# Optimization experiments

Measured on AMD Instinct MI355X. Metric: run time of the kernel, lower is better.

Reference implementation:

```python
import jax, jax.numpy as jnp
import numpy as np

B, S, E, H, FF = 4, 1024, 1024, 16, 4096
D = E // H
EPS = 1e-5


def layer_norm(x, g, b):
    m = jnp.mean(x, axis=-1, keepdims=True)
    v = jnp.var(x, axis=-1, keepdims=True)
    return (x - m) / jnp.sqrt(v + EPS) * g + b


def setup_inputs() -> dict:
    key = jax.random.key(0)
    ks = jax.random.split(key, 12)
    x = jax.random.normal(ks[0], (B, S, E), dtype=jnp.float32)
    # binary attention mask [B,S,S]; force diagonal=1 so no row is fully masked
    mask = jax.random.randint(ks[1], (B, S, S), 0, 2).astype(jnp.float32)
    idx = jnp.arange(S)
    mask = mask.at[:, idx, idx].set(1.0)
    gnn_adj = jax.random.normal(ks[2], (B, S, S), dtype=jnp.float32) * 0.02
    sc = 0.02
    params = dict(
        Wq=jax.random.normal(ks[3], (E, E), dtype=jnp.float32) * sc, bq=jnp.zeros((E,), jnp.float32),
        Wk=jax.random.normal(ks[4], (E, E), dtype=jnp.float32) * sc, bk=jnp.zeros((E,), jnp.float32),
        Wv=jax.random.normal(ks[5], (E, E), dtype=jnp.float32) * sc, bv=jnp.zeros((E,), jnp.float32),
        Wo=jax.random.normal(ks[6], (E, E), dtype=jnp.float32) * sc, bo=jnp.zeros((E,), jnp.float32),
        g1=jnp.ones((E,), jnp.float32), b1=jnp.zeros((E,), jnp.float32),
        g2=jnp.ones((E,), jnp.float32), b2=jnp.zeros((E,), jnp.float32),
        W1=jax.random.normal(ks[7], (E, FF), dtype=jnp.float32) * sc, bf1=jnp.zeros((FF,), jnp.float32),
        W2=jax.random.normal(ks[8], (FF, E), dtype=jnp.float32) * sc, bf2=jnp.zeros((E,), jnp.float32),
    )
    return dict(x=x, mask=mask, gnn_adj=gnn_adj, **params)


def reference(x, mask, gnn_adj, Wq, bq, Wk, bk, Wv, bv, Wo, bo, g1, b1, g2, b2, W1, bf1, W2, bf2):
    # pre-norm (norm_first=True), dropout = identity (eval)
    nx = layer_norm(x, g1, b1)
    # QKV projections -> [B,H,S,D]
    def split_heads(t):
        return t.reshape(B, S, H, D).transpose(0, 2, 1, 3)
    q = split_heads(nx @ Wq + bq)
    k = split_heads(nx @ Wk + bk)
    v = split_heads(nx @ Wv + bv)
    scores = jnp.einsum('bhqd,bhkd->bhqk', q, k) / jnp.sqrt(jnp.float32(D))
    m = mask[:, None]  # [B,1,S,S]
    scores = jnp.where(m == 0, -jnp.inf, scores * m)
    attn = jax.nn.softmax(scores, axis=-1)
    # non-standard: additive bias AFTER softmax
    attn = attn + gnn_adj[:, None]
    xv = jnp.einsum('bhqk,bhkd->bhqd', attn, v)
    xv = xv.transpose(0, 2, 1, 3).reshape(B, S, E)
    x = x + (xv @ Wo + bo)
    h = layer_norm(x, g2, b2)
    ff = jax.nn.gelu(h @ W1 + bf1, approximate=False) @ W2 + bf2
    return x + ff
```

## Files before the change

### kernel.cpp

```cpp
#include <hip/hip_runtime.h>
#include <hip/hip_bf16.h>

typedef unsigned short u16;
typedef short bf16x8 __attribute__((ext_vector_type(8)));
typedef float f32x4 __attribute__((ext_vector_type(4)));

#define B_ 4
#define S_ 1024
#define E_ 1024
#define H_ 16
#define FF_ 4096
#define D_ 64
#define M_ 4096

__device__ __forceinline__ u16 f2bf(float f) {
  unsigned int u = __builtin_bit_cast(unsigned int, f);
  u += 0x7fffu + ((u >> 16) & 1u);
  return (u16)(u >> 16);
}
__device__ __forceinline__ float bf2f(u16 v) {
  unsigned int u = ((unsigned int)v) << 16;
  return __builtin_bit_cast(float, u);
}

__device__ __forceinline__ void gld_lds16(const void* g, void* l) {
  __builtin_amdgcn_global_load_lds((__attribute__((address_space(1))) void*)g,
                                   (__attribute__((address_space(3))) void*)l,
                                   16, 0, 0);
}

__global__ void __launch_bounds__(256) pre_kernel(
    const float* __restrict__ wq, const float* __restrict__ wk,
    const float* __restrict__ wv, const float* __restrict__ wo,
    const float* __restrict__ w1, const float* __restrict__ w2,
    u16* __restrict__ wt,
    const float* __restrict__ x, const float* __restrict__ g1,
    const float* __restrict__ b1, u16* __restrict__ nx,
    const float* __restrict__ mask, const float* __restrict__ gnn,
    u16* __restrict__ biasI, u16* __restrict__ gnnbf) {
  __shared__ __attribute__((aligned(16))) float smem_f[1088];
  int bid = blockIdx.x;
  int t = threadIdx.x;
  if (bid < 12288) {
    const float* src; u16* dst; int K, N; int local;
    if (bid < 4096) {
      int wsel = bid >> 10; local = bid & 1023; K = 1024; N = 1024;
      src = wsel == 0 ? wq : wsel == 1 ? wk : wsel == 2 ? wv : wo;
      dst = wt + (size_t)wsel * 1024 * 1024;
    } else if (bid < 8192) {
      local = bid - 4096; K = 1024; N = 4096; src = w1;
      dst = wt + (size_t)4 * 1024 * 1024;
    } else {
      local = bid - 8192; K = 4096; N = 1024; src = w2;
      dst = wt + (size_t)8 * 1024 * 1024;
    }
    int tiles_n = N >> 5;
    int n0 = (local % tiles_n) << 5, k0 = (local / tiles_n) << 5;
    float (*tl)[33] = reinterpret_cast<float(*)[33]>(smem_f);
    int tx = t & 31, ty = t >> 5;
#pragma unroll
    for (int i = 0; i < 4; ++i)
      tl[ty + i * 8][tx] = src[(size_t)(k0 + ty + i * 8) * N + n0 + tx];
    __syncthreads();
#pragma unroll
    for (int i = 0; i < 4; ++i)
      dst[(size_t)(n0 + ty + i * 8) * K + k0 + tx] = f2bf(tl[tx][ty + i * 8]);
  } else if (bid < 16384) {
    int row = bid - 12288;
    const float* xr = x + (size_t)row * 1024;
    float4 v = *(const float4*)(xr + t * 4);
    float s = v.x + v.y + v.z + v.w;
    float q = v.x * v.x + v.y * v.y + v.z * v.z + v.w * v.w;
#pragma unroll
    for (int off = 1; off < 64; off <<= 1) {
      s += __shfl_xor(s, off);
      q += __shfl_xor(q, off);
    }
    float* sb = smem_f;
    float* qb = smem_f + 4;
    int w = t >> 6, l = t & 63;
    if (l == 0) { sb[w] = s; qb[w] = q; }
    __syncthreads();
    s = sb[0] + sb[1] + sb[2] + sb[3];
    q = qb[0] + qb[1] + qb[2] + qb[3];
    float mean = s * (1.f / 1024.f);
    float var = q * (1.f / 1024.f) - mean * mean;
    float rs = rsqrtf(var + 1e-5f);
    float4 gv = *(const float4*)(g1 + t * 4);
    float4 bv = *(const float4*)(b1 + t * 4);
    ushort4 o;
    o.x = f2bf((v.x - mean) * rs * gv.x + bv.x);
    o.y = f2bf((v.y - mean) * rs * gv.y + bv.y);
    o.z = f2bf((v.z - mean) * rs * gv.z + bv.z);
    o.w = f2bf((v.w - mean) * rs * gv.w + bv.w);
    *(ushort4*)(nx + (size_t)row * 1024 + t * 4) = o;
  } else {
    int row = bid - 16384;
    int b = row >> 10, q = row & 1023;
    float* mrow = smem_f;
    const float* mp = mask + ((size_t)row << 10);
    const float* gp = gnn + ((size_t)row << 10);
    float4 mv = *(const float4*)(mp + t * 4);
    *(float4*)(mrow + t * 4) = mv;
    float4 gv = *(const float4*)(gp + t * 4);
    ushort4 g4;
    g4.x = f2bf(gv.x); g4.y = f2bf(gv.y); g4.z = f2bf(gv.z); g4.w = f2bf(gv.w);
    *(ushort4*)(gnnbf + ((size_t)row << 10) + t * 4) = g4;
    __syncthreads();
    int kt = t >> 4, c = t & 15;
    const u16 NEG = f2bf(-30008.f);
    const u16 SHIFT = f2bf(-8.0f);
    ushort4 o;
    o.x = (mrow[kt * 64 + c] == 0.f) ? NEG : SHIFT;
    o.y = (mrow[kt * 64 + 16 + c] == 0.f) ? NEG : SHIFT;
    o.z = (mrow[kt * 64 + 32 + c] == 0.f) ? NEG : SHIFT;
    o.w = (mrow[kt * 64 + 48 + c] == 0.f) ? NEG : SHIFT;
    *(ushort4*)(biasI + (((size_t)(b * 16 + kt) << 10) + q) * 64 + c * 4) = o;
  }
}

__global__ void __launch_bounds__(256) vtrans_kernel(
    const u16* __restrict__ v, u16* __restrict__ vt) {
  int st = blockIdx.x, h = blockIdx.y, b = blockIdx.z;
  __shared__ u16 tl[64][72];
  const u16* src = v + ((((size_t)(b * 16 + h)) << 10) + (st << 6)) * 64;
  int r = threadIdx.x >> 2, g = (threadIdx.x & 3) << 4;
  *(uint4*)&tl[r][g] = *(const uint4*)(src + r * 64 + g);
  *(uint4*)&tl[r][g + 8] = *(const uint4*)(src + r * 64 + g + 8);
  __syncthreads();
  u16 tmp[16];
#pragma unroll
  for (int i = 0; i < 16; ++i) tmp[i] = tl[g + i][r];
  u16* dst = vt + ((size_t)b << 20) + (((size_t)(h * 64 + r)) << 10) + (st << 6) + g;
  *(uint4*)(dst) = *(uint4*)(tmp);
  *(uint4*)(dst + 8) = *(uint4*)(tmp + 8);
}

__global__ void __launch_bounds__(256) ln_kernel_b(
    const u16* __restrict__ x, const float* __restrict__ g,
    const float* __restrict__ bt, u16* __restrict__ out) {
  int row = blockIdx.x, t = threadIdx.x;
  const u16* xr = x + ((size_t)row << 10);
  ushort4 xv4 = *(const ushort4*)(xr + t * 4);
  float v0 = bf2f(xv4.x), v1 = bf2f(xv4.y), v2 = bf2f(xv4.z), v3 = bf2f(xv4.w);
  float s = v0 + v1 + v2 + v3;
  float q = v0 * v0 + v1 * v1 + v2 * v2 + v3 * v3;
#pragma unroll
  for (int off = 1; off < 64; off <<= 1) {
    s += __shfl_xor(s, off);
    q += __shfl_xor(q, off);
  }
  __shared__ float sb[4], qb[4];
  int w = t >> 6, l = t & 63;
  if (l == 0) { sb[w] = s; qb[w] = q; }
  __syncthreads();
  s = sb[0] + sb[1] + sb[2] + sb[3];
  q = qb[0] + qb[1] + qb[2] + qb[3];
  float mean = s * (1.f / 1024.f);
  float var = q * (1.f / 1024.f) - mean * mean;
  float rs = rsqrtf(var + 1e-5f);
  float4 gv = *(const float4*)(g + t * 4);
  float4 bv = *(const float4*)(bt + t * 4);
  ushort4 o;
  o.x = f2bf((v0 - mean) * rs * gv.x + bv.x);
  o.y = f2bf((v1 - mean) * rs * gv.y + bv.y);
  o.z = f2bf((v2 - mean) * rs * gv.z + bv.z);
  o.w = f2bf((v3 - mean) * rs * gv.w + bv.w);
  *(ushort4*)(out + ((size_t)row << 10) + t * 4) = o;
}

template <int LDA, int LDB, int NKT>
__device__ __forceinline__ void gemm_core_db64(
    const u16* __restrict__ A, const u16* __restrict__ Bt,
    int bm, int bn, u16* lds, f32x4 acc[4][2]) {
  const int tid = threadIdx.x;
  const int w = tid >> 6, l = tid & 63;
  const int wn = w << 5;
  const int lrow = l >> 3;
  const int cg = (l & 7) ^ lrow;
  const u16* Ab = A + (size_t)(bm << 6) * LDA + (cg << 3);
  const u16* Bb = Bt + (size_t)(bn << 7) * LDB + (cg << 3);
#define GSTAGE64(T, BUF)                                                     \
  {                                                                          \
    const int kk = (T) << 6;                                                 \
    u16* la = lds + (BUF) * 12288;                                           \
    u16* lb = la + 4096;                                                     \
    _Pragma("unroll") for (int i = 0; i < 2; ++i) {                          \
      int c = (w << 1) + i;                                                  \
      int row = (c << 3) + lrow;                                             \
      gld_lds16(Ab + (size_t)row * LDA + kk, la + (c << 9));                 \
    }                                                                        \
    _Pragma("unroll") for (int i = 0; i < 4; ++i) {                          \
      int c = (w << 2) + i;                                                  \
      int row = (c << 3) + lrow;                                             \
      gld_lds16(Bb + (size_t)row * LDB + kk, lb + (c << 9));                 \
    }                                                                        \
  }
  GSTAGE64(0, 0);
  __syncthreads();
  for (int t = 0; t < NKT; ++t) {
    if (t + 1 < NKT) GSTAGE64(t + 1, (t & 1) ^ 1);
    const u16* la = lds + (t & 1) * 12288;
    const u16* lb = la + 4096;
    bf16x8 af[2][4], bfr[2][2];
    const int rr = l & 15;
    const int kgb = l >> 4;
#pragma unroll
    for (int ks = 0; ks < 2; ++ks) {
      const int kg = kgb + (ks << 2);
#pragma unroll
      for (int f = 0; f < 4; ++f) {
        int ra = (f << 4) + rr;
        af[ks][f] = *(const bf16x8*)(la + (ra << 6) + ((kg ^ (ra & 7)) << 3));
      }
#pragma unroll
      for (int f = 0; f < 2; ++f) {
        int rb = wn + (f << 4) + rr;
        bfr[ks][f] = *(const bf16x8*)(lb + (rb << 6) + ((kg ^ (rb & 7)) << 3));
      }
    }
#pragma unroll
    for (int fm = 0; fm < 4; ++fm)
#pragma unroll
      for (int fn = 0; fn < 2; ++fn)
#pragma unroll
        for (int ks = 0; ks < 2; ++ks)
          acc[fm][fn] = __builtin_amdgcn_mfma_f32_16x16x32_bf16(
              af[ks][fm], bfr[ks][fn], acc[fm][fn], 0, 0, 0);
    __syncthreads();
  }
#undef GSTAGE64
}

#define ACC_INIT64()                      \
  f32x4 acc[4][2];                        \
  { f32x4 zf = {0.f, 0.f, 0.f, 0.f};      \
_Pragma("unroll")                         \
    for (int a = 0; a < 4; ++a)           \
_Pragma("unroll")                         \
      for (int bb = 0; bb < 2; ++bb) acc[a][bb] = zf; }

#define EPI_SETUP64()                                   \
  const int w = threadIdx.x >> 6, l = threadIdx.x & 63; \
  const int wn = w << 5;

#define GEMM_LDS64() __shared__ __attribute__((aligned(16))) u16 lds[2 * 12288]

__global__ void __launch_bounds__(256, 2) gemm_qkv(
    const u16* __restrict__ nx, const u16* __restrict__ wt,
    const float* __restrict__ bq, const float* __restrict__ bk,
    const float* __restrict__ bv, u16* __restrict__ qk, u16* __restrict__ vtmp) {
  GEMM_LDS64();
  ACC_INIT64();
  int z = blockIdx.z;
  const u16* Bt = wt + (size_t)z * 1024 * 1024;
  const float* bias = z == 0 ? bq : z == 1 ? bk : bv;
  u16* out = z == 2 ? vtmp : qk + (size_t)z * M_ * 1024;
  const float scl = (z == 0) ? 0.18033688f : 1.0f;
  gemm_core_db64<1024, 1024, 16>(nx, Bt, blockIdx.x, blockIdx.y, lds, acc);
  EPI_SETUP64();
#pragma unroll
  for (int fm = 0; fm < 4; ++fm)
#pragma unroll
    for (int fn = 0; fn < 2; ++fn)
#pragma unroll
      for (int j = 0; j < 4; ++j) {
        int row = (blockIdx.x << 6) + (fm << 4) + ((l >> 4) << 2) + j;
        int col = (blockIdx.y << 7) + wn + (fn << 4) + (l & 15);
        float v = (acc[fm][fn][j] + bias[col]) * scl;
        int b = row >> 10, s = row & 1023;
        int h = col >> 6, d = col & 63;
        out[(((size_t)(b * 16 + h) << 10) + s) * 64 + d] = f2bf(v);
      }
}

__global__ void __launch_bounds__(256, 2) gemm_gnnv(
    const u16* __restrict__ gnnbf, const u16* __restrict__ vt,
    u16* __restrict__ xvg) {
  GEMM_LDS64();
  ACC_INIT64();
  int b = blockIdx.z;
  const u16* A = gnnbf + ((size_t)b << 20);
  const u16* Bt = vt + ((size_t)b << 20);
  u16* out = xvg + ((size_t)b << 20);
  gemm_core_db64<1024, 1024, 16>(A, Bt, blockIdx.x, blockIdx.y, lds, acc);
  EPI_SETUP64();
#pragma unroll
  for (int fm = 0; fm < 4; ++fm)
#pragma unroll
    for (int fn = 0; fn < 2; ++fn)
#pragma unroll
      for (int j = 0; j < 4; ++j) {
        int row = (blockIdx.x << 6) + (fm << 4) + ((l >> 4) << 2) + j;
        int col = (blockIdx.y << 7) + wn + (fn << 4) + (l & 15);
        out[((size_t)row << 10) + col] = f2bf(acc[fm][fn][j]);
      }
}

__global__ void __launch_bounds__(256, 2) gemm_wo(
    const u16* __restrict__ xv, const u16* __restrict__ wt,
    const float* __restrict__ bo, const float* __restrict__ xres,
    u16* __restrict__ x1b) {
  GEMM_LDS64();
  ACC_INIT64();
  gemm_core_db64<1024, 1024, 16>(xv, wt, blockIdx.x, blockIdx.y, lds, acc);
  EPI_SETUP64();
#pragma unroll
  for (int fm = 0; fm < 4; ++fm)
#pragma unroll
    for (int fn = 0; fn < 2; ++fn)
#pragma unroll
      for (int j = 0; j < 4; ++j) {
        int row = (blockIdx.x << 6) + (fm << 4) + ((l >> 4) << 2) + j;
        int col = (blockIdx.y << 7) + wn + (fn << 4) + (l & 15);
        size_t idx = ((size_t)row << 10) + col;
        x1b[idx] = f2bf(acc[fm][fn][j] + bo[col] + xres[idx]);
      }
}

__global__ void __launch_bounds__(256, 2) gemm_w1(
    const u16* __restrict__ hb, const u16* __restrict__ wt,
    const float* __restrict__ bf1, u16* __restrict__ ff1) {
  GEMM_LDS64();
  ACC_INIT64();
  gemm_core_db64<1024, 1024, 16>(hb, wt, blockIdx.x, blockIdx.y, lds, acc);
  EPI_SETUP64();
#pragma unroll
  for (int fm = 0; fm < 4; ++fm)
#pragma unroll
    for (int fn = 0; fn < 2; ++fn)
#pragma unroll
      for (int j = 0; j < 4; ++j) {
        int row = (blockIdx.x << 6) + (fm << 4) + ((l >> 4) << 2) + j;
        int col = (blockIdx.y << 7) + wn + (fn << 4) + (l & 15);
        float v = acc[fm][fn][j] + bf1[col];
        float ge = 0.5f * v * (1.f + erff(v * 0.70710678118654752f));
        ff1[((size_t)row << 12) + col] = f2bf(ge);
      }
}

__global__ void __launch_bounds__(256, 2) gemm_w2(
    const u16* __restrict__ ff1, const u16* __restrict__ wt,
    const float* __restrict__ bf2, const u16* __restrict__ x1b,
    float* __restrict__ out) {
  GEMM_LDS64();
  ACC_INIT64();
  gemm_core_db64<4096, 4096, 64>(ff1, wt, blockIdx.x, blockIdx.y, lds, acc);
  EPI_SETUP64();
#pragma unroll
  for (int fm = 0; fm < 4; ++fm)
#pragma unroll
    for (int fn = 0; fn < 2; ++fn)
#pragma unroll
      for (int j = 0; j < 4; ++j) {
        int row = (blockIdx.x << 6) + (fm << 4) + ((l >> 4) << 2) + j;
        int col = (blockIdx.y << 7) + wn + (fn << 4) + (l & 15);
        size_t idx = ((size_t)row << 10) + col;
        out[idx] = acc[fm][fn][j] + bf2[col] + bf2f(x1b[idx]);
      }
}

__global__ void __launch_bounds__(256, 2) attn_kernel(
    const u16* __restrict__ Q, const u16* __restrict__ K,
    const u16* __restrict__ Vt, const u16* __restrict__ biasI,
    const u16* __restrict__ xvg, u16* __restrict__ xv) {
  const int lin = ((blockIdx.x & 7) << 6) + (blockIdx.x >> 3);
  const int qt = lin & 7, h = (lin >> 3) & 15, b = lin >> 7;
  const int tid = threadIdx.x, w = tid >> 6, l = tid & 63;
  __shared__ __attribute__((aligned(16))) u16 kbuf[2][64 * 64];
  __shared__ __attribute__((aligned(16))) u16 vbuf[2][64 * 64];
  __shared__ __attribute__((aligned(16))) u16 pbuf[4][32 * 64];
  const size_t bh = ((size_t)(b * 16 + h)) << 16;
  const u16* Qb = Q + bh;
  const u16* Kb = K + bh;
  const u16* Vtb = Vt + ((size_t)b << 20) + ((size_t)(h * 64) << 10);
  const u16* biasb = biasI + ((size_t)b << 20);
  const int q0 = (qt << 7) + (w << 5);
  const int lrow = l >> 3, cg = (l & 7) ^ lrow;
  const int l4 = l >> 4, lo = l & 15;
  u16* p_w = pbuf[w];

  bf16x8 qf[2][2];
#pragma unroll
  for (int m = 0; m < 2; ++m)
#pragma unroll
    for (int ks = 0; ks < 2; ++ks)
      qf[m][ks] = *(const bf16x8*)(Qb + ((size_t)(q0 + m * 16 + lo) << 6) +
                                   l4 * 8 + ks * 32);
  bf16x8 onesf;
#pragma unroll
  for (int j = 0; j < 8; ++j) onesf[j] = (short)0x3F80;

  f32x4 osoft[2][4], osum[2];
  f32x4 zf = {0.f, 0.f, 0.f, 0.f};
#pragma unroll
  for (int m = 0; m < 2; ++m) {
    osum[m] = zf;
#pragma unroll
    for (int fd = 0; fd < 4; ++fd) osoft[m][fd] = zf;
  }

#define STAGE(T, BUF)                                                          \
  {                                                                            \
    int kv0s = (T) << 6;                                                       \
    u16* kd = &kbuf[BUF][0];                                                   \
    u16* vd = &vbuf[BUF][0];                                                   \
    _Pragma("unroll") for (int i = 0; i < 2; ++i) {                            \
      int c = (w << 1) + i;                                                    \
      gld_lds16(Kb + ((size_t)(kv0s + (c << 3) + lrow) << 6) + (cg << 3),      \
                kd + (c << 9));                                                \
      gld_lds16(Vtb + ((size_t)((c << 3) + lrow) << 10) + kv0s + (cg << 3),    \
                vd + (c << 9));                                                \
    }                                                                          \
  }

  STAGE(0, 0);
  __syncthreads();

  for (int t = 0; t < 16; ++t) {
    const int cur = t & 1;
    if (t < 15) STAGE(t + 1, cur ^ 1);
    const u16* kb_ = &kbuf[cur][0];
    const u16* vb_ = &vbuf[cur][0];
    f32x4 sacc[2][4];
#pragma unroll
    for (int m = 0; m < 2; ++m)
#pragma unroll
      for (int j = 0; j < 4; ++j) {
        ushort4 bb = *(const ushort4*)(
            biasb + (((size_t)(t * 1024 + q0 + m * 16 + l4 * 4 + j)) << 6) +
            lo * 4);
        sacc[m][0][j] = bf2f(bb.x);
        sacc[m][1][j] = bf2f(bb.y);
        sacc[m][2][j] = bf2f(bb.z);
        sacc[m][3][j] = bf2f(bb.w);
      }
    __builtin_amdgcn_s_setprio(1);
#pragma unroll
    for (int ks = 0; ks < 2; ++ks) {
      const int kg = l4 + (ks << 2);
      bf16x8 kf[4];
#pragma unroll
      for (int fn = 0; fn < 4; ++fn) {
        int rk = (fn << 4) + lo;
        kf[fn] = *(const bf16x8*)(kb_ + (rk << 6) + ((kg ^ (rk & 7)) << 3));
      }
#pragma unroll
      for (int m = 0; m < 2; ++m)
#pragma unroll
        for (int fn = 0; fn < 4; ++fn)
          sacc[m][fn] = __builtin_amdgcn_mfma_f32_16x16x32_bf16(
              qf[m][ks], kf[fn], sacc[m][fn], 0, 0, 0);
    }
    __builtin_amdgcn_s_setprio(0);
#pragma unroll
    for (int m = 0; m < 2; ++m)
#pragma unroll
      for (int fn = 0; fn < 4; ++fn)
#pragma unroll
        for (int j = 0; j < 4; ++j) {
          float p = exp2f(sacc[m][fn][j]);
          unsigned int u = __builtin_bit_cast(unsigned int, p);
          int prow = (m << 4) + (l4 << 2) + j;
          int pcol = (fn << 4) + lo;
          p_w[(prow << 6) + (pcol ^ ((prow & 7) << 3))] =
              (u16)((u + 0x8000u) >> 16);
        }
    __builtin_amdgcn_s_setprio(1);
#pragma unroll
    for (int ks = 0; ks < 2; ++ks) {
      const int kg = l4 + (ks << 2);
      bf16x8 pf[2], vf[4];
#pragma unroll
      for (int m = 0; m < 2; ++m) {
        int pr = (m << 4) + lo;
        pf[m] = *(const bf16x8*)(p_w + (pr << 6) + ((kg ^ (pr & 7)) << 3));
      }
#pragma unroll
      for (int fd = 0; fd < 4; ++fd) {
        int rd = (fd << 4) + lo;
        vf[fd] = *(const bf16x8*)(vb_ + (rd << 6) + ((kg ^ (rd & 7)) << 3));
      }
#pragma unroll
      for (int m = 0; m < 2; ++m) {
        osum[m] = __builtin_amdgcn_mfma_f32_16x16x32_bf16(
            pf[m], onesf, osum[m], 0, 0, 0);
#pragma unroll
        for (int fd = 0; fd < 4; ++fd)
          osoft[m][fd] = __builtin_amdgcn_mfma_f32_16x16x32_bf16(
              pf[m], vf[fd], osoft[m][fd], 0, 0, 0);
      }
    }
    __builtin_amdgcn_s_setprio(0);
    __syncthreads();
  }
#pragma unroll
  for (int m = 0; m < 2; ++m) {
    f32x4 rl;
#pragma unroll
    for (int j = 0; j < 4; ++j) rl[j] = 1.0f / osum[m][j];
#pragma unroll
    for (int fd = 0; fd < 4; ++fd)
#pragma unroll
      for (int j = 0; j < 4; ++j) {
        int qrow = q0 + (m << 4) + (l4 << 2) + j;
        int e = (h << 6) + (fd << 4) + lo;
        size_t idx = (((size_t)(b * 1024 + qrow)) << 10) + e;
        float o = osoft[m][fd][j] * rl[j] + bf2f(xvg[idx]);
        xv[idx] = f2bf(o);
      }
  }
#undef STAGE
}

extern "C" void kernel_launch(void* const* d_in, const int* in_sizes, int n_in,
                              void* d_out, int out_size, void* d_ws, size_t ws_size,
                              hipStream_t stream) {
  (void)in_sizes; (void)n_in; (void)out_size; (void)ws_size;
  const float* x   = (const float*)d_in[0];
  const float* mask= (const float*)d_in[1];
  const float* gnn = (const float*)d_in[2];
  const float* Wq  = (const float*)d_in[3];
  const float* bq  = (const float*)d_in[4];
  const float* Wk  = (const float*)d_in[5];
  const float* bk  = (const float*)d_in[6];
  const float* Wv  = (const float*)d_in[7];
  const float* bv  = (const float*)d_in[8];
  const float* Wo  = (const float*)d_in[9];
  const float* bo  = (const float*)d_in[10];
  const float* g1  = (const float*)d_in[11];
  const float* b1  = (const float*)d_in[12];
  const float* g2  = (const float*)d_in[13];
  const float* b2  = (const float*)d_in[14];
  const float* W1  = (const float*)d_in[15];
  const float* bf1 = (const float*)d_in[16];
  const float* W2  = (const float*)d_in[17];
  const float* bf2 = (const float*)d_in[18];
  float* out = (float*)d_out;

  char* ws = (char*)d_ws;
  const size_t MB = 1024 * 1024;
  u16*  wt    = (u16*)(ws);
  u16*  nx    = (u16*)(ws + 24 * MB);
  u16*  xvbuf = (u16*)(ws + 24 * MB);
  u16*  hbuf  = (u16*)(ws + 24 * MB);
  u16*  qk    = (u16*)(ws + 32 * MB);
  u16*  vt    = (u16*)(ws + 48 * MB);
  u16*  biasI = (u16*)(ws + 56 * MB);
  u16*  gnnbf = (u16*)(ws + 64 * MB);
  u16*  x1b   = (u16*)(ws + 64 * MB);
  u16*  vtmp  = (u16*)(ws + 72 * MB);
  u16*  xvg   = (u16*)(ws + 72 * MB);
  u16*  ff1   = (u16*)(ws + 32 * MB);

  pre_kernel<<<20480, 256, 0, stream>>>(Wq, Wk, Wv, Wo, W1, W2, wt,
                                        x, g1, b1, nx, mask, gnn, biasI, gnnbf);
  gemm_qkv<<<dim3(64, 8, 3), 256, 0, stream>>>(nx, wt, bq, bk, bv, qk, vtmp);
  vtrans_kernel<<<dim3(16, 16, 4), 256, 0, stream>>>(vtmp, vt);
  gemm_gnnv<<<dim3(16, 8, 4), 256, 0, stream>>>(gnnbf, vt, xvg);
  attn_kernel<<<512, 256, 0, stream>>>(
      qk, qk + (size_t)4 * MB, vt, biasI, xvg, xvbuf);
  gemm_wo<<<dim3(64, 8), 256, 0, stream>>>(xvbuf, wt + (size_t)3 * MB, bo, x, x1b);
  ln_kernel_b<<<4096, 256, 0, stream>>>(x1b, g2, b2, hbuf);
  gemm_w1<<<dim3(64, 32), 256, 0, stream>>>(hbuf, wt + (size_t)4 * MB, bf1, ff1);
  gemm_w2<<<dim3(64, 8), 256, 0, stream>>>(ff1, wt + (size_t)8 * MB, bf2, x1b, out);
}
```

Baseline: 230.7 us.

## Use 256x256 tiles with 512 threads for the W1 FFN GEMM

Replaces the 64x128-tile W1 GEMM with a new kernel that computes 256x256 output tiles using 8 waves. Each wave holds a 128x64 accumulator and the kernel uses a swizzled LDS layout, K-steps of 32 and grid-order remapping for L2 locality. The larger tile raises arithmetic intensity and cuts global and LDS traffic per FLOP. The cost is 256 blocks on a 256-CU part (one wave of blocks), much higher register pressure, and only one block per CU.

```diff
diff --git a/kernel.cpp b/kernel.cpp
--- a/kernel.cpp
+++ b/kernel.cpp
@@ -244,7 +244,7 @@
   const int w = threadIdx.x >> 6, l = threadIdx.x & 63; \
   const int wn = w << 5;
 
-#define GEMM_LDS64() __shared__ __attribute__((aligned(16))) u16 lds[2 * 12288]
+#define GEMM_LDS64()  __shared__ __attribute__((aligned(16))) u16 lds[2 * 12288]
 
 __global__ void __launch_bounds__(256, 2) gemm_qkv(
     const u16* __restrict__ nx, const u16* __restrict__ wt,
@@ -318,21 +318,82 @@
       }
 }
 
-__global__ void __launch_bounds__(256, 2) gemm_w1(
+__global__ void __launch_bounds__(512, 1) gemm_w1_256(
     const u16* __restrict__ hb, const u16* __restrict__ wt,
     const float* __restrict__ bf1, u16* __restrict__ ff1) {
-  GEMM_LDS64();
-  ACC_INIT64();
-  gemm_core_db64<1024, 1024, 16>(hb, wt, blockIdx.x, blockIdx.y, lds, acc);
-  EPI_SETUP64();
-#pragma unroll
-  for (int fm = 0; fm < 4; ++fm)
-#pragma unroll
-    for (int fn = 0; fn < 2; ++fn)
+  __shared__ __attribute__((aligned(16))) u16 lds[2 * 16384];
+  const int bid = blockIdx.x;
+  const int lin = ((bid & 7) << 5) + (bid >> 3);
+  const int bm = lin & 15, bn = lin >> 4;
+  const int tid = threadIdx.x;
+  const int w = tid >> 6, l = tid & 63;
+  const int wm = (w >> 2) << 7;
+  const int wn = (w & 3) << 6;
+  const int lrow3 = l >> 3;
+  const int vsw = (l & 7) ^ lrow3;
+  const int rpar = vsw >> 2, k8s = vsw & 3;
+  const u16* Ab = hb + (size_t)(bm << 8) * 1024 + k8s * 8;
+  const u16* Bb = wt + (size_t)(bn << 8) * 1024 + k8s * 8;
+
+  f32x4 acc[8][4];
+  {
+    f32x4 zf = {0.f, 0.f, 0.f, 0.f};
+#pragma unroll
+    for (int a = 0; a < 8; ++a)
+#pragma unroll
+      for (int bb2 = 0; bb2 < 4; ++bb2) acc[a][bb2] = zf;
+  }
+
+#define GSTAGE256(T, BUF)                                                    \
+  {                                                                          \
+    const int kk = (T) << 5;                                                 \
+    u16* la = lds + (BUF) * 16384;                                           \
+    u16* lb = la + 8192;                                                     \
+    _Pragma("unroll") for (int i = 0; i < 2; ++i) {                          \
+      int c = (w << 1) + i;                                       \
+      int row = ((c << 3) + lrow3) * 2 + rpar;                               \
+      gld_lds16(Ab + (size_t)row * 1024 + kk, la + (c << 9) + (l << 3));     \
+      gld_lds16(Bb + (size_t)row * 1024 + kk, lb + (c << 9) + (l << 3));     \
+    }                                                                        \
+  }
+
+  GSTAGE256(0, 0);
+  __syncthreads();
+
+  const int rr = l & 15;
+  const int kg = l >> 4;
+  for (int t = 0; t < 32; ++t) {
+    if (t + 1 < 32) GSTAGE256(t + 1, (t & 1) ^ 1);
+    const u16* la = lds + (t & 1) * 16384;
+    const u16* lb = la + 8192;
+    bf16x8 bfr[4];
+#pragma unroll
+    for (int fn = 0; fn < 4; ++fn) {
+      int rb = wn + (fn << 4) + rr;
+      int slot = (((rb & 1) << 2) | kg) ^ ((rb >> 1) & 7);
+      bfr[fn] = *(const bf16x8*)(lb + ((rb >> 1) << 6) + (slot << 3));
+    }
+#pragma unroll
+    for (int fm = 0; fm < 8; ++fm) {
+      int ra = wm + (fm << 4) + rr;
+      int slot = (((ra & 1) << 2) | kg) ^ ((ra >> 1) & 7);
+      bf16x8 afr = *(const bf16x8*)(la + ((ra >> 1) << 6) + (slot << 3));
+#pragma unroll
+      for (int fn = 0; fn < 4; ++fn)
+        acc[fm][fn] = __builtin_amdgcn_mfma_f32_16x16x32_bf16(
+            afr, bfr[fn], acc[fm][fn], 0, 0, 0);
+    }
+    __syncthreads();
+  }
+#undef GSTAGE256
+#pragma unroll
+  for (int fm = 0; fm < 8; ++fm)
+#pragma unroll
+    for (int fn = 0; fn < 4; ++fn)
 #pragma unroll
       for (int j = 0; j < 4; ++j) {
-        int row = (blockIdx.x << 6) + (fm << 4) + ((l >> 4) << 2) + j;
-        int col = (blockIdx.y << 7) + wn + (fn << 4) + (l & 15);
+        int row = (bm << 8) + wm + (fm << 4) + ((l >> 4) << 2) + j;
+        int col = (bn << 8) + wn + (fn << 4) + (l & 15);
         float v = acc[fm][fn][j] + bf1[col];
         float ge = 0.5f * v * (1.f + erff(v * 0.70710678118654752f));
         ff1[((size_t)row << 12) + col] = f2bf(ge);
@@ -562,6 +623,6 @@
       qk, qk + (size_t)4 * MB, vt, biasI, xvg, xvbuf);
   gemm_wo<<<dim3(64, 8), 256, 0, stream>>>(xvbuf, wt + (size_t)3 * MB, bo, x, x1b);
   ln_kernel_b<<<4096, 256, 0, stream>>>(x1b, g2, b2, hbuf);
-  gemm_w1<<<dim3(64, 32), 256, 0, stream>>>(hbuf, wt + (size_t)4 * MB, bf1, ff1);
+  gemm_w1_256<<<256, 512, 0, stream>>>(hbuf, wt + (size_t)4 * MB, bf1, ff1);
   gemm_w2<<<dim3(64, 8), 256, 0, stream>>>(ff1, wt + (size_t)8 * MB, bf2, x1b, out);
 }
```

New measurement: 231.9 us. Within noise of the previous version (+0.5%).
